# Performance work log

Measured on AMD Instinct MI355X. Metric: run time of the kernel, lower is better.

The kernel has to match this reference:

```python
import jax, jax.numpy as jnp
import numpy as np

N_NODES = 100000
IN_CH, HID_CH, OUT_CH = 128, 256, 128
N_EDGES = 1600000


def setup_inputs() -> dict:
    key = jax.random.key(0)
    ks = jax.random.split(key, 12)
    x = jax.random.normal(ks[0], (N_NODES, IN_CH), dtype=jnp.float32)
    edge_index = jax.random.randint(ks[1], (2, N_EDGES), 0, N_NODES, dtype=jnp.int32)
    s1 = 1.0 / np.sqrt(IN_CH)
    s2 = 1.0 / np.sqrt(HID_CH)
    return {
        "x": x,
        "edge_index": edge_index,
        "eps1": jnp.zeros((), jnp.float32),
        "W1a": jax.random.uniform(ks[2], (IN_CH, HID_CH), jnp.float32, -s1, s1),
        "b1a": jax.random.uniform(ks[3], (HID_CH,), jnp.float32, -s1, s1),
        "W1b": jax.random.uniform(ks[4], (HID_CH, HID_CH), jnp.float32, -s2, s2),
        "b1b": jax.random.uniform(ks[5], (HID_CH,), jnp.float32, -s2, s2),
        "eps2": jnp.zeros((), jnp.float32),
        "W2a": jax.random.uniform(ks[6], (HID_CH, HID_CH), jnp.float32, -s2, s2),
        "b2a": jax.random.uniform(ks[7], (HID_CH,), jnp.float32, -s2, s2),
        "W2b": jax.random.uniform(ks[8], (HID_CH, OUT_CH), jnp.float32, -s2, s2),
        "b2b": jax.random.uniform(ks[9], (OUT_CH,), jnp.float32, -s2, s2),
    }


def _gin_conv(x, src, dst, eps, Wa, ba, Wb, bb):
    # sum-aggregate source features into destinations: [N, d]
    agg = jax.ops.segment_sum(x[src], dst, num_segments=N_NODES)
    h = (1.0 + eps) * x + agg
    h = jax.nn.relu(h @ Wa + ba)
    return h @ Wb + bb


def reference(x, edge_index, eps1, W1a, b1a, W1b, b1b, eps2, W2a, b2a, W2b, b2b):
    src, dst = edge_index[0], edge_index[1]
    h = _gin_conv(x, src, dst, eps1, W1a, b1a, W1b, b1b)
    h = jax.nn.relu(h)
    out = _gin_conv(h, src, dst, eps2, W2a, b2a, W2b, b2b)
    return out
```

## Files before the change

### kernel.cpp

```cpp
#include <hip/hip_runtime.h>

#define N_NODES 100000
#define N_EDGES 1600000
#define NB 782
#define SC_BLK 256

typedef __attribute__((ext_vector_type(8))) short short8;
typedef __attribute__((ext_vector_type(4))) float float4e;

#define GLDS16(g, l)                                                   \
  __builtin_amdgcn_global_load_lds(                                    \
      (const __attribute__((address_space(1))) unsigned int*)(g),      \
      (__attribute__((address_space(3))) unsigned int*)(l), 16, 0, 0)

__device__ __forceinline__ unsigned short f2bf(float f) {
  unsigned u = __float_as_uint(f);
  u += 0x7FFFu + ((u >> 16) & 1u);
  return (unsigned short)(u >> 16);
}
__device__ __forceinline__ float bf2f(unsigned short h) {
  return __uint_as_float(((unsigned)h) << 16);
}

__global__ __launch_bounds__(256) void histA_k(const int* __restrict__ dst,
                                               int* __restrict__ bh, int nE) {
  __shared__ int h[NB];
  const int blk = blockIdx.x, tid = threadIdx.x;
  for (int b = tid; b < NB; b += 256) h[b] = 0;
  __syncthreads();
  const int epb = (nE + SC_BLK - 1) / SC_BLK;
  const int i1 = min(blk * epb + epb, nE);
  for (int i = blk * epb + tid; i < i1; i += 256)
    atomicAdd(&h[dst[i] >> 7], 1);
  __syncthreads();
  for (int b = tid; b < NB; b += 256) bh[b * SC_BLK + blk] = h[b];
}

__global__ __launch_bounds__(256) void scanW_k(int* __restrict__ bh,
                                               int* __restrict__ tot) {
  const int b = blockIdx.x * 4 + (threadIdx.x >> 6);
  const int lane = threadIdx.x & 63;
  if (b >= NB) return;
  const int base = b * SC_BLK + lane * 4;
  int v[4];
#pragma unroll
  for (int j = 0; j < 4; ++j) v[j] = bh[base + j];
  int ls = v[0] + v[1] + v[2] + v[3];
  int x = ls;
  for (int off = 1; off < 64; off <<= 1) {
    int y = __shfl_up(x, off);
    if (lane >= off) x += y;
  }
  int run = x - ls;
#pragma unroll
  for (int j = 0; j < 4; ++j) {
    int t = v[j];
    bh[base + j] = run;
    run += t;
  }
  if (lane == 63) tot[b] = run;
}

__global__ __launch_bounds__(1024) void scanB2_k(const int* __restrict__ tot,
                                                 int* __restrict__ bucketStart) {
  __shared__ int sm[1024];
  const int tid = threadIdx.x;
  int v = (tid < NB) ? tot[tid] : 0;
  sm[tid] = v;
  __syncthreads();
  for (int off = 1; off < 1024; off <<= 1) {
    int t = (tid >= off) ? sm[tid - off] : 0;
    __syncthreads();
    sm[tid] += t;
    __syncthreads();
  }
  if (tid < NB) bucketStart[tid] = sm[tid] - v;
  if (tid == NB - 1) bucketStart[NB] = sm[tid];
}

__global__ __launch_bounds__(256) void scatter2_k(
    const int* __restrict__ src, const int* __restrict__ dst,
    const int* __restrict__ bucketStart, const int* __restrict__ bh,
    unsigned int* __restrict__ packed, int nE) {
  __shared__ int cur[NB];
  const int blk = blockIdx.x, tid = threadIdx.x;
  for (int b = tid; b < NB; b += 256)
    cur[b] = bucketStart[b] + bh[b * SC_BLK + blk];
  __syncthreads();
  const int epb = (nE + SC_BLK - 1) / SC_BLK;
  const int i1 = min(blk * epb + epb, nE);
  for (int i = blk * epb + tid; i < i1; i += 256) {
    int d = dst[i];
    int s = src[i];
    int p = atomicAdd(&cur[d >> 7], 1);
    packed[p] = ((unsigned)s << 7) | (unsigned)(d & 127);
  }
}

__global__ __launch_bounds__(256) void fillB_k(
    const int* __restrict__ bucketStart, const unsigned int* __restrict__ packed,
    int* __restrict__ rowEnd, int* __restrict__ sortedSrc, int nNodes) {
  __shared__ int cnt[128];
  __shared__ int cur[128];
  const int b = blockIdx.x;
  const int tid = threadIdx.x;
  const int s0 = bucketStart[b];
  const int ne = bucketStart[b + 1] - s0;
  if (tid < 128) cnt[tid] = 0;
  __syncthreads();
  for (int i = tid; i < ne; i += 256)
    atomicAdd(&cnt[packed[s0 + i] & 127u], 1);
  __syncthreads();
  int v = (tid < 128) ? cnt[tid] : 0;
  for (int off = 1; off < 128; off <<= 1) {
    int t = (tid < 128 && tid >= off) ? cnt[tid - off] : 0;
    __syncthreads();
    if (tid < 128) cnt[tid] += t;
    __syncthreads();
  }
  if (tid < 128) {
    cur[tid] = s0 + cnt[tid] - v;
    int node = b * 128 + tid;
    if (node < nNodes) rowEnd[node] = s0 + cnt[tid];
  }
  __syncthreads();
  for (int i = tid; i < ne; i += 256) {
    unsigned p = packed[s0 + i];
    int idx = atomicAdd(&cur[p & 127u], 1);
    sortedSrc[idx] = (int)(p >> 7);
  }
}

__global__ __launch_bounds__(256) void wprep_k(
    const float* __restrict__ W, unsigned short* __restrict__ th,
    unsigned short* __restrict__ tl, int K, int N) {
  int i = blockIdx.x * blockDim.x + threadIdx.x;
  if (i < K * N) {
    int k = i / N, n = i % N;
    float v = W[i];
    unsigned short h = f2bf(v);
    unsigned short l = f2bf(v - bf2f(h));
    th[(long)n * K + k] = h;
    tl[(long)n * K + k] = l;
  }
}

__global__ __launch_bounds__(256) void xprep_k(const float* __restrict__ x,
                                               unsigned short* __restrict__ xh,
                                               int n) {
  int i = blockIdx.x * blockDim.x + threadIdx.x;
  if (i < n) xh[i] = f2bf(x[i]);
}

template <bool XF32>
__global__ __launch_bounds__(256) void agg_s_k(
    const unsigned short* __restrict__ feat_h, const float* __restrict__ xf,
    const unsigned short* __restrict__ xh, const unsigned short* __restrict__ xl,
    const float* __restrict__ epsp, const int* __restrict__ rowEnd,
    const int* __restrict__ sortedSrc, unsigned short* __restrict__ oh,
    unsigned short* __restrict__ ol, int M, int S, int off) {
  constexpr int V = 2;
  const int lane = threadIdx.x & 63;
  const int w = (int)((blockIdx.x * blockDim.x + threadIdx.x) >> 6);
  if (w >= M) return;
  const int start = w ? rowEnd[w - 1] : 0;
  const int end = rowEnd[w];
  const int c0 = lane * V + off;

  float acc[V] = {};
  int e = start;
  for (; e + 8 <= end; e += 8) {
    int si[8];
#pragma unroll
    for (int q = 0; q < 8; ++q) si[q] = sortedSrc[e + q];
    ushort2 t[8];
#pragma unroll
    for (int q = 0; q < 8; ++q)
      t[q] = *(const ushort2*)(feat_h + (long)si[q] * S + c0);
#pragma unroll
    for (int q = 0; q < 8; ++q) {
      acc[0] += bf2f(t[q].x);
      acc[1] += bf2f(t[q].y);
    }
  }
  for (; e + 4 <= end; e += 4) {
    int s0 = sortedSrc[e + 0];
    int s1 = sortedSrc[e + 1];
    int s2 = sortedSrc[e + 2];
    int s3 = sortedSrc[e + 3];
    ushort2 a = *(const ushort2*)(feat_h + (long)s0 * S + c0);
    ushort2 b = *(const ushort2*)(feat_h + (long)s1 * S + c0);
    ushort2 c = *(const ushort2*)(feat_h + (long)s2 * S + c0);
    ushort2 d = *(const ushort2*)(feat_h + (long)s3 * S + c0);
    acc[0] += bf2f(a.x) + bf2f(b.x) + bf2f(c.x) + bf2f(d.x);
    acc[1] += bf2f(a.y) + bf2f(b.y) + bf2f(c.y) + bf2f(d.y);
  }
  for (; e < end; ++e) {
    ushort2 a = *(const ushort2*)(feat_h + (long)sortedSrc[e] * S + c0);
    acc[0] += bf2f(a.x);
    acc[1] += bf2f(a.y);
  }

  const float s = 1.0f + epsp[0];
  float xv[V];
  if constexpr (XF32) {
#pragma unroll
    for (int v = 0; v < V; ++v) xv[v] = xf[(long)w * S + c0 + v];
  } else {
#pragma unroll
    for (int v = 0; v < V; ++v)
      xv[v] = bf2f(xh[(long)w * S + c0 + v]) + bf2f(xl[(long)w * S + c0 + v]);
  }

  unsigned short hv[V], lv[V];
#pragma unroll
  for (int v = 0; v < V; ++v) {
    float res = fmaf(s, xv[v], acc[v]);
    hv[v] = f2bf(res);
    lv[v] = f2bf(res - bf2f(hv[v]));
  }
  *(ushort2*)&oh[(long)w * S + c0] = make_ushort2(hv[0], hv[1]);
  *(ushort2*)&ol[(long)w * S + c0] = make_ushort2(lv[0], lv[1]);
}

__device__ __forceinline__ short8 lds_rd(const unsigned short* base, int r,
                                         int q) {
  int L = r * 64 + q * 16;
  int P = L ^ (((L >> 7) & 7) << 4);
  return *(const short8*)((const char*)base + P);
}

template <bool RELU, bool HILO>
__global__ __launch_bounds__(256, 2) void gemm128_k(
    const unsigned short* __restrict__ Ah, const unsigned short* __restrict__ Al,
    const unsigned short* __restrict__ Bth, const unsigned short* __restrict__ Btl,
    const float* __restrict__ bias, float* __restrict__ outf,
    unsigned short* __restrict__ oh, unsigned short* __restrict__ ol,
    int M, int K, int NOUT) {
  __shared__ unsigned short Ash[128 * 32];
  __shared__ unsigned short Asl[128 * 32];
  __shared__ unsigned short Bsh[128 * 32];
  __shared__ unsigned short Bsl[128 * 32];

  const int tid = threadIdx.x;
  const int lane = tid & 63;
  const int wave = tid >> 6;
  const int l15 = lane & 15;
  const int quad = lane >> 4;
  const int wm = wave >> 1;
  const int wn = wave & 1;
  const int m0 = blockIdx.x * 128;
  const int n0 = blockIdx.y * 128;

  float4e acc[4][4];
#pragma unroll
  for (int i = 0; i < 4; ++i)
#pragma unroll
    for (int j = 0; j < 4; ++j) acc[i][j] = 0.0f;

  for (int k0 = 0; k0 < K; k0 += 32) {
#pragma unroll
    for (int h = 0; h < 2; ++h) {
      int c = h * 256 + tid;
      int P = c * 16;
      int L = P ^ (((P >> 7) & 7) << 4);
      int r = L >> 6;
      int q = (L >> 4) & 3;
      if (m0 + r < M) {
        long ga = (long)(m0 + r) * K + k0 + q * 8;
        GLDS16(Ah + ga, Ash + c * 8);
        GLDS16(Al + ga, Asl + c * 8);
      }
      long gb = (long)(n0 + r) * K + k0 + q * 8;
      GLDS16(Bth + gb, Bsh + c * 8);
      GLDS16(Btl + gb, Bsl + c * 8);
    }
    __syncthreads();

    short8 ah[4], al[4];
#pragma unroll
    for (int mi = 0; mi < 4; ++mi) {
      ah[mi] = lds_rd(Ash, wm * 64 + mi * 16 + l15, quad);
      al[mi] = lds_rd(Asl, wm * 64 + mi * 16 + l15, quad);
    }
#pragma unroll
    for (int ni = 0; ni < 4; ++ni) {
      short8 bh = lds_rd(Bsh, wn * 64 + ni * 16 + l15, quad);
      short8 bl = lds_rd(Bsl, wn * 64 + ni * 16 + l15, quad);
#pragma unroll
      for (int mi = 0; mi < 4; ++mi) {
        acc[mi][ni] =
            __builtin_amdgcn_mfma_f32_16x16x32_bf16(ah[mi], bh, acc[mi][ni], 0, 0, 0);
        acc[mi][ni] =
            __builtin_amdgcn_mfma_f32_16x16x32_bf16(ah[mi], bl, acc[mi][ni], 0, 0, 0);
        acc[mi][ni] =
            __builtin_amdgcn_mfma_f32_16x16x32_bf16(al[mi], bh, acc[mi][ni], 0, 0, 0);
      }
    }
    __syncthreads();
  }

#pragma unroll
  for (int mi = 0; mi < 4; ++mi) {
#pragma unroll
    for (int ni = 0; ni < 4; ++ni) {
      int col = n0 + wn * 64 + ni * 16 + l15;
      float bj = bias[col];
      int rbase = m0 + wm * 64 + mi * 16 + quad * 4;
#pragma unroll
      for (int r = 0; r < 4; ++r) {
        int row = rbase + r;
        if (row < M) {
          float v = acc[mi][ni][r] + bj;
          if constexpr (RELU) v = fmaxf(v, 0.0f);
          if constexpr (HILO) {
            unsigned short h = f2bf(v);
            oh[(long)row * NOUT + col] = h;
            ol[(long)row * NOUT + col] = f2bf(v - bf2f(h));
          } else {
            outf[(long)row * NOUT + col] = v;
          }
        }
      }
    }
  }
}

extern "C" void kernel_launch(void* const* d_in, const int* in_sizes, int n_in,
                              void* d_out, int out_size, void* d_ws, size_t ws_size,
                              hipStream_t stream) {
  const float* x    = (const float*)d_in[0];
  const int*   ei   = (const int*)d_in[1];
  const float* eps1 = (const float*)d_in[2];
  const float* W1a  = (const float*)d_in[3];
  const float* b1a  = (const float*)d_in[4];
  const float* W1b  = (const float*)d_in[5];
  const float* b1b  = (const float*)d_in[6];
  const float* eps2 = (const float*)d_in[7];
  const float* W2a  = (const float*)d_in[8];
  const float* b2a  = (const float*)d_in[9];
  const float* W2b  = (const float*)d_in[10];
  const float* b2b  = (const float*)d_in[11];
  float* out = (float*)d_out;

  const int* srcp = ei;
  const int* dstp = ei + N_EDGES;

  char* ws = (char*)d_ws;
  const size_t SZ = (size_t)N_NODES * 256 * sizeof(float);
  char* P1 = ws;
  char* P2 = ws + SZ;

  unsigned short* C1h = (unsigned short*)P1;
  unsigned short* C1l = C1h + (size_t)N_NODES * 128;
  unsigned short* xh  = C1l + (size_t)N_NODES * 128;
  unsigned short* T1h = (unsigned short*)P2;
  unsigned short* T1l = T1h + (size_t)N_NODES * 256;
  unsigned short* Hh = (unsigned short*)P1;
  unsigned short* Hl = Hh + (size_t)N_NODES * 256;
  unsigned short* C2h = (unsigned short*)P2;
  unsigned short* C2l = C2h + (size_t)N_NODES * 256;
  unsigned short* T2h = (unsigned short*)P1;
  unsigned short* T2l = T2h + (size_t)N_NODES * 256;
  unsigned short* W2bh = (unsigned short*)P2;
  unsigned short* W2bl = W2bh + 128 * 256;

  char* ob = (char*)d_out;
  int* rowEnd    = (int*)(ob + 400 * 1024);
  int* sortedSrc = (int*)(ob + 800 * 1024);
  size_t wofs = 7340032;
  unsigned short* W1ah = (unsigned short*)(ob + wofs);
  unsigned short* W1al = W1ah + 256 * 128;
  unsigned short* W1bh = (unsigned short*)(ob + wofs + 2 * 65536);
  unsigned short* W1bl = W1bh + 256 * 256;
  unsigned short* W2ah = (unsigned short*)(ob + wofs + 2 * 65536 + 2 * 131072);
  unsigned short* W2al = W2ah + 256 * 256;
  unsigned int* packed = (unsigned int*)(ob + 16 * 1024 * 1024);
  int* bucketStart = (int*)(ob + 28 * 1024 * 1024);
  int* bucketTot   = (int*)(ob + 28 * 1024 * 1024 + 8192);
  int* blockHist   = (int*)(ob + 30 * 1024 * 1024);

  dim3 blk(256);
  dim3 gAgg((N_NODES + 3) / 4);
  dim3 gW1((128 * 256 + 255) / 256);
  dim3 gW2((256 * 256 + 255) / 256);
  dim3 gXp((N_NODES * 128 + 255) / 256);
  dim3 gGemm2((N_NODES + 127) / 128, 2);
  dim3 gGemm1((N_NODES + 127) / 128, 1);

  histA_k<<<dim3(SC_BLK), blk, 0, stream>>>(dstp, blockHist, N_EDGES);
  scanW_k<<<dim3((NB + 3) / 4), blk, 0, stream>>>(blockHist, bucketTot);
  scanB2_k<<<1, dim3(1024), 0, stream>>>(bucketTot, bucketStart);
  scatter2_k<<<dim3(SC_BLK), blk, 0, stream>>>(srcp, dstp, bucketStart,
                                               blockHist, packed, N_EDGES);
  fillB_k<<<dim3(NB), blk, 0, stream>>>(bucketStart, packed, rowEnd, sortedSrc,
                                        N_NODES);
  xprep_k<<<gXp, blk, 0, stream>>>(x, xh, N_NODES * 128);
  wprep_k<<<gW1, blk, 0, stream>>>(W1a, W1ah, W1al, 128, 256);
  wprep_k<<<gW2, blk, 0, stream>>>(W1b, W1bh, W1bl, 256, 256);
  wprep_k<<<gW2, blk, 0, stream>>>(W2a, W2ah, W2al, 256, 256);

  agg_s_k<true><<<gAgg, blk, 0, stream>>>(
      xh, x, nullptr, nullptr, eps1, rowEnd, sortedSrc, C1h, C1l, N_NODES, 128, 0);
  gemm128_k<true, true><<<gGemm2, blk, 0, stream>>>(
      C1h, C1l, W1ah, W1al, b1a, nullptr, T1h, T1l, N_NODES, 128, 256);
  gemm128_k<true, true><<<gGemm2, blk, 0, stream>>>(
      T1h, T1l, W1bh, W1bl, b1b, nullptr, Hh, Hl, N_NODES, 256, 256);

  agg_s_k<false><<<gAgg, blk, 0, stream>>>(
      Hh, nullptr, Hh, Hl, eps2, rowEnd, sortedSrc, C2h, C2l, N_NODES, 256, 0);
  agg_s_k<false><<<gAgg, blk, 0, stream>>>(
      Hh, nullptr, Hh, Hl, eps2, rowEnd, sortedSrc, C2h, C2l, N_NODES, 256, 128);
  gemm128_k<true, true><<<gGemm2, blk, 0, stream>>>(
      C2h, C2l, W2ah, W2al, b2a, nullptr, T2h, T2l, N_NODES, 256, 256);
  wprep_k<<<gW1, blk, 0, stream>>>(W2b, W2bh, W2bl, 256, 128);
  gemm128_k<false, false><<<gGemm1, blk, 0, stream>>>(
      T2h, T2l, W2bh, W2bl, b2b, out, nullptr, nullptr, N_NODES, 256, 128);
}
```

Baseline: 662.7 us.

## Double-buffer GEMM LDS tiles to overlap global loads with MFMA

The GEMM kernel now keeps two LDS buffers per operand and issues the global-to-LDS loads for the next K tile before computing on the current one, using explicit vmcnt waits and raw barriers. The goal is to hide global load latency behind the bf16 hi/lo MFMA work. Out-of-range A rows are clamped instead of skipped so every thread issues the same number of loads, which keeps the vmcnt count fixed. The cost is twice the LDS (64KB per block), which may lower occupancy against the launch_bounds(256,2) target, and it relies on the hand-written waitcnt being correct.

```diff
diff --git a/kernel.cpp b/kernel.cpp
--- a/kernel.cpp
+++ b/kernel.cpp
@@ -12,6 +12,9 @@
   __builtin_amdgcn_global_load_lds(                                    \
       (const __attribute__((address_space(1))) unsigned int*)(g),      \
       (__attribute__((address_space(3))) unsigned int*)(l), 16, 0, 0)
+
+#define WAITVM_(N) asm volatile("s_waitcnt vmcnt(" #N ")" ::: "memory")
+#define WAITVM(N) WAITVM_(N)
 
 __device__ __forceinline__ unsigned short f2bf(float f) {
   unsigned u = __float_as_uint(f);
@@ -237,10 +240,10 @@
     const float* __restrict__ bias, float* __restrict__ outf,
     unsigned short* __restrict__ oh, unsigned short* __restrict__ ol,
     int M, int K, int NOUT) {
-  __shared__ unsigned short Ash[128 * 32];
-  __shared__ unsigned short Asl[128 * 32];
-  __shared__ unsigned short Bsh[128 * 32];
-  __shared__ unsigned short Bsl[128 * 32];
+  __shared__ unsigned short Ash[2][128 * 32];
+  __shared__ unsigned short Asl[2][128 * 32];
+  __shared__ unsigned short Bsh[2][128 * 32];
+  __shared__ unsigned short Bsl[2][128 * 32];
 
   const int tid = threadIdx.x;
   const int lane = tid & 63;
@@ -258,7 +261,7 @@
 #pragma unroll
     for (int j = 0; j < 4; ++j) acc[i][j] = 0.0f;
 
-  for (int k0 = 0; k0 < K; k0 += 32) {
+  auto stage = [&](int buf, int k0) {
 #pragma unroll
     for (int h = 0; h < 2; ++h) {
       int c = h * 256 + tid;
@@ -266,27 +269,40 @@
       int L = P ^ (((P >> 7) & 7) << 4);
       int r = L >> 6;
       int q = (L >> 4) & 3;
-      if (m0 + r < M) {
-        long ga = (long)(m0 + r) * K + k0 + q * 8;
-        GLDS16(Ah + ga, Ash + c * 8);
-        GLDS16(Al + ga, Asl + c * 8);
-      }
+      int ra = min(m0 + r, M - 1);
+      long ga = (long)ra * K + k0 + q * 8;
+      GLDS16(Ah + ga, &Ash[buf][c * 8]);
+      GLDS16(Al + ga, &Asl[buf][c * 8]);
       long gb = (long)(n0 + r) * K + k0 + q * 8;
-      GLDS16(Bth + gb, Bsh + c * 8);
-      GLDS16(Btl + gb, Bsl + c * 8);
-    }
-    __syncthreads();
+      GLDS16(Bth + gb, &Bsh[buf][c * 8]);
+      GLDS16(Btl + gb, &Bsl[buf][c * 8]);
+    }
+  };
+
+  const int nt = K >> 5;
+  stage(0, 0);
+
+  for (int t = 0; t < nt; ++t) {
+    const int cur = t & 1;
+    if (t + 1 < nt) {
+      stage(cur ^ 1, (t + 1) * 32);
+      WAITVM(8);
+    } else {
+      WAITVM(0);
+    }
+    __builtin_amdgcn_s_barrier();
+    __builtin_amdgcn_sched_barrier(0);
 
     short8 ah[4], al[4];
 #pragma unroll
     for (int mi = 0; mi < 4; ++mi) {
-      ah[mi] = lds_rd(Ash, wm * 64 + mi * 16 + l15, quad);
-      al[mi] = lds_rd(Asl, wm * 64 + mi * 16 + l15, quad);
+      ah[mi] = lds_rd(&Ash[cur][0], wm * 64 + mi * 16 + l15, quad);
+      al[mi] = lds_rd(&Asl[cur][0], wm * 64 + mi * 16 + l15, quad);
     }
 #pragma unroll
     for (int ni = 0; ni < 4; ++ni) {
-      short8 bh = lds_rd(Bsh, wn * 64 + ni * 16 + l15, quad);
-      short8 bl = lds_rd(Bsl, wn * 64 + ni * 16 + l15, quad);
+      short8 bh = lds_rd(&Bsh[cur][0], wn * 64 + ni * 16 + l15, quad);
+      short8 bl = lds_rd(&Bsl[cur][0], wn * 64 + ni * 16 + l15, quad);
 #pragma unroll
       for (int mi = 0; mi < 4; ++mi) {
         acc[mi][ni] =
@@ -297,7 +313,8 @@
             __builtin_amdgcn_mfma_f32_16x16x32_bf16(al[mi], bh, acc[mi][ni], 0, 0, 0);
       }
     }
-    __syncthreads();
+    __builtin_amdgcn_s_barrier();
+    __builtin_amdgcn_sched_barrier(0);
   }
 
 #pragma unroll
```

New measurement: 718.1 us. 1.08x slower.

## Fuse each GIN MLP's two GEMMs into one kernel keeping hidden tile in LDS

Applied to the files above, without the earlier changes.

Each pair of back-to-back GEMMs in a GIN MLP now runs as one kernel. The 128x256 hidden tile is written as hi/lo bf16 into LDS and consumed directly by the second GEMM, so the T1/T2 intermediates no longer round-trip through global memory and two launches are removed. Weights are now read straight from global memory (through cache) instead of being staged in LDS. The kernel uses about 144KB of LDS at one block per CU, which lowers occupancy and may stall on the uncoalesced per-lane weight loads.

```diff
diff --git a/kernel.cpp b/kernel.cpp
--- a/kernel.cpp
+++ b/kernel.cpp
@@ -230,17 +230,22 @@
   return *(const short8*)((const char*)base + P);
 }
 
-template <bool RELU, bool HILO>
-__global__ __launch_bounds__(256, 2) void gemm128_k(
+#define MFMA_BF16 __builtin_amdgcn_mfma_f32_16x16x32_bf16
+
+template <int K1, int NF2, bool RELU2, bool HILO2>
+__global__ __launch_bounds__(256, 1) void gemm_fused_k(
     const unsigned short* __restrict__ Ah, const unsigned short* __restrict__ Al,
-    const unsigned short* __restrict__ Bth, const unsigned short* __restrict__ Btl,
-    const float* __restrict__ bias, float* __restrict__ outf,
-    unsigned short* __restrict__ oh, unsigned short* __restrict__ ol,
-    int M, int K, int NOUT) {
+    const unsigned short* __restrict__ B1th, const unsigned short* __restrict__ B1tl,
+    const float* __restrict__ bias1,
+    const unsigned short* __restrict__ B2th, const unsigned short* __restrict__ B2tl,
+    const float* __restrict__ bias2,
+    float* __restrict__ outf, unsigned short* __restrict__ oh,
+    unsigned short* __restrict__ ol, int M) {
+  constexpr int N2 = NF2 * 32;
   __shared__ unsigned short Ash[128 * 32];
   __shared__ unsigned short Asl[128 * 32];
-  __shared__ unsigned short Bsh[128 * 32];
-  __shared__ unsigned short Bsl[128 * 32];
+  __shared__ unsigned short Th[8 * 128 * 32];
+  __shared__ unsigned short Tl[8 * 128 * 32];
 
   const int tid = threadIdx.x;
   const int lane = tid & 63;
@@ -250,75 +255,119 @@
   const int wm = wave >> 1;
   const int wn = wave & 1;
   const int m0 = blockIdx.x * 128;
-  const int n0 = blockIdx.y * 128;
-
-  float4e acc[4][4];
+
+  {
+    float4e acc1[4][8];
+#pragma unroll
+    for (int i = 0; i < 4; ++i)
+#pragma unroll
+      for (int j = 0; j < 8; ++j) acc1[i][j] = 0.0f;
+
+    for (int k0 = 0; k0 < K1; k0 += 32) {
+#pragma unroll
+      for (int h = 0; h < 2; ++h) {
+        int c = h * 256 + tid;
+        int P = c * 16;
+        int L = P ^ (((P >> 7) & 7) << 4);
+        int r = L >> 6;
+        int q = (L >> 4) & 3;
+        int ra = min(m0 + r, M - 1);
+        long ga = (long)ra * K1 + k0 + q * 8;
+        GLDS16(Ah + ga, &Ash[c * 8]);
+        GLDS16(Al + ga, &Asl[c * 8]);
+      }
+      __syncthreads();
+
+      short8 ah[4], al[4];
+#pragma unroll
+      for (int mi = 0; mi < 4; ++mi) {
+        ah[mi] = lds_rd(Ash, wm * 64 + mi * 16 + l15, quad);
+        al[mi] = lds_rd(Asl, wm * 64 + mi * 16 + l15, quad);
+      }
+#pragma unroll
+      for (int ni = 0; ni < 8; ++ni) {
+        int n = wn * 128 + ni * 16 + l15;
+        short8 bh = *(const short8*)(B1th + (long)n * K1 + k0 + quad * 8);
+        short8 bl = *(const short8*)(B1tl + (long)n * K1 + k0 + quad * 8);
+#pragma unroll
+        for (int mi = 0; mi < 4; ++mi) {
+          acc1[mi][ni] = MFMA_BF16(ah[mi], bh, acc1[mi][ni], 0, 0, 0);
+          acc1[mi][ni] = MFMA_BF16(ah[mi], bl, acc1[mi][ni], 0, 0, 0);
+          acc1[mi][ni] = MFMA_BF16(al[mi], bh, acc1[mi][ni], 0, 0, 0);
+        }
+      }
+      __syncthreads();
+    }
+
+#pragma unroll
+    for (int ni = 0; ni < 8; ++ni) {
+      int col = wn * 128 + ni * 16 + l15;
+      float bj = bias1[col];
+      int sb = (col >> 5) * 4096;
+      int c5 = (col & 31) * 2;
+#pragma unroll
+      for (int mi = 0; mi < 4; ++mi) {
+#pragma unroll
+        for (int r = 0; r < 4; ++r) {
+          int row = wm * 64 + mi * 16 + quad * 4 + r;
+          float v = fmaxf(acc1[mi][ni][r] + bj, 0.0f);
+          unsigned short hv = f2bf(v);
+          unsigned short lv = f2bf(v - bf2f(hv));
+          int L = row * 64 + c5;
+          int P = L ^ (((L >> 7) & 7) << 4);
+          *(unsigned short*)((char*)(Th + sb) + P) = hv;
+          *(unsigned short*)((char*)(Tl + sb) + P) = lv;
+        }
+      }
+    }
+  }
+  __syncthreads();
+
+  float4e acc2[4][NF2];
 #pragma unroll
   for (int i = 0; i < 4; ++i)
 #pragma unroll
-    for (int j = 0; j < 4; ++j) acc[i][j] = 0.0f;
-
-  for (int k0 = 0; k0 < K; k0 += 32) {
-#pragma unroll
-    for (int h = 0; h < 2; ++h) {
-      int c = h * 256 + tid;
-      int P = c * 16;
-      int L = P ^ (((P >> 7) & 7) << 4);
-      int r = L >> 6;
-      int q = (L >> 4) & 3;
-      if (m0 + r < M) {
-        long ga = (long)(m0 + r) * K + k0 + q * 8;
-        GLDS16(Ah + ga, Ash + c * 8);
-        GLDS16(Al + ga, Asl + c * 8);
-      }
-      long gb = (long)(n0 + r) * K + k0 + q * 8;
-      GLDS16(Bth + gb, Bsh + c * 8);
-      GLDS16(Btl + gb, Bsl + c * 8);
-    }
-    __syncthreads();
-
-    short8 ah[4], al[4];
+    for (int j = 0; j < NF2; ++j) acc2[i][j] = 0.0f;
+
+  for (int kt = 0; kt < 8; ++kt) {
+    short8 ah2[4], al2[4];
 #pragma unroll
     for (int mi = 0; mi < 4; ++mi) {
-      ah[mi] = lds_rd(Ash, wm * 64 + mi * 16 + l15, quad);
-      al[mi] = lds_rd(Asl, wm * 64 + mi * 16 + l15, quad);
-    }
-#pragma unroll
-    for (int ni = 0; ni < 4; ++ni) {
-      short8 bh = lds_rd(Bsh, wn * 64 + ni * 16 + l15, quad);
-      short8 bl = lds_rd(Bsl, wn * 64 + ni * 16 + l15, quad);
+      ah2[mi] = lds_rd(Th + kt * 4096, wm * 64 + mi * 16 + l15, quad);
+      al2[mi] = lds_rd(Tl + kt * 4096, wm * 64 + mi * 16 + l15, quad);
+    }
+#pragma unroll
+    for (int ni = 0; ni < NF2; ++ni) {
+      int n = wn * (NF2 * 16) + ni * 16 + l15;
+      short8 bh = *(const short8*)(B2th + (long)n * 256 + kt * 32 + quad * 8);
+      short8 bl = *(const short8*)(B2tl + (long)n * 256 + kt * 32 + quad * 8);
 #pragma unroll
       for (int mi = 0; mi < 4; ++mi) {
-        acc[mi][ni] =
-            __builtin_amdgcn_mfma_f32_16x16x32_bf16(ah[mi], bh, acc[mi][ni], 0, 0, 0);
-        acc[mi][ni] =
-            __builtin_amdgcn_mfma_f32_16x16x32_bf16(ah[mi], bl, acc[mi][ni], 0, 0, 0);
-        acc[mi][ni] =
-            __builtin_amdgcn_mfma_f32_16x16x32_bf16(al[mi], bh, acc[mi][ni], 0, 0, 0);
-      }
-    }
-    __syncthreads();
-  }
-
-#pragma unroll
-  for (int mi = 0; mi < 4; ++mi) {
-#pragma unroll
-    for (int ni = 0; ni < 4; ++ni) {
-      int col = n0 + wn * 64 + ni * 16 + l15;
-      float bj = bias[col];
-      int rbase = m0 + wm * 64 + mi * 16 + quad * 4;
+        acc2[mi][ni] = MFMA_BF16(ah2[mi], bh, acc2[mi][ni], 0, 0, 0);
+        acc2[mi][ni] = MFMA_BF16(ah2[mi], bl, acc2[mi][ni], 0, 0, 0);
+        acc2[mi][ni] = MFMA_BF16(al2[mi], bh, acc2[mi][ni], 0, 0, 0);
+      }
+    }
+  }
+
+#pragma unroll
+  for (int ni = 0; ni < NF2; ++ni) {
+    int col = wn * (NF2 * 16) + ni * 16 + l15;
+    float bj = bias2[col];
+#pragma unroll
+    for (int mi = 0; mi < 4; ++mi) {
 #pragma unroll
       for (int r = 0; r < 4; ++r) {
-        int row = rbase + r;
+        int row = m0 + wm * 64 + mi * 16 + quad * 4 + r;
         if (row < M) {
-          float v = acc[mi][ni][r] + bj;
-          if constexpr (RELU) v = fmaxf(v, 0.0f);
-          if constexpr (HILO) {
-            unsigned short h = f2bf(v);
-            oh[(long)row * NOUT + col] = h;
-            ol[(long)row * NOUT + col] = f2bf(v - bf2f(h));
+          float v = acc2[mi][ni][r] + bj;
+          if constexpr (RELU2) v = fmaxf(v, 0.0f);
+          if constexpr (HILO2) {
+            unsigned short hv = f2bf(v);
+            oh[(long)row * N2 + col] = hv;
+            ol[(long)row * N2 + col] = f2bf(v - bf2f(hv));
           } else {
-            outf[(long)row * NOUT + col] = v;
+            outf[(long)row * N2 + col] = v;
           }
         }
       }
@@ -354,15 +403,13 @@
   unsigned short* C1h = (unsigned short*)P1;
   unsigned short* C1l = C1h + (size_t)N_NODES * 128;
   unsigned short* xh  = C1l + (size_t)N_NODES * 128;
-  unsigned short* T1h = (unsigned short*)P2;
-  unsigned short* T1l = T1h + (size_t)N_NODES * 256;
-  unsigned short* Hh = (unsigned short*)P1;
-  unsigned short* Hl = Hh + (size_t)N_NODES * 256;
-  unsigned short* C2h = (unsigned short*)P2;
+  unsigned short* Hh  = (unsigned short*)P2;
+  unsigned short* Hl  = Hh + (size_t)N_NODES * 256;
+  unsigned short* C2h = (unsigned short*)P1;
   unsigned short* C2l = C2h + (size_t)N_NODES * 256;
-  unsigned short* T2h = (unsigned short*)P1;
-  unsigned short* T2l = T2h + (size_t)N_NODES * 256;
-  unsigned short* W2bh = (unsigned short*)P2;
+  unsigned short* W2ah = (unsigned short*)P2;
+  unsigned short* W2al = W2ah + 256 * 256;
+  unsigned short* W2bh = W2al + 256 * 256;
   unsigned short* W2bl = W2bh + 128 * 256;
 
   char* ob = (char*)d_out;
@@ -373,8 +420,6 @@
   unsigned short* W1al = W1ah + 256 * 128;
   unsigned short* W1bh = (unsigned short*)(ob + wofs + 2 * 65536);
   unsigned short* W1bl = W1bh + 256 * 256;
-  unsigned short* W2ah = (unsigned short*)(ob + wofs + 2 * 65536 + 2 * 131072);
-  unsigned short* W2al = W2ah + 256 * 256;
   unsigned int* packed = (unsigned int*)(ob + 16 * 1024 * 1024);
   int* bucketStart = (int*)(ob + 28 * 1024 * 1024);
   int* bucketTot   = (int*)(ob + 28 * 1024 * 1024 + 8192);
@@ -385,8 +430,7 @@
   dim3 gW1((128 * 256 + 255) / 256);
   dim3 gW2((256 * 256 + 255) / 256);
   dim3 gXp((N_NODES * 128 + 255) / 256);
-  dim3 gGemm2((N_NODES + 127) / 128, 2);
-  dim3 gGemm1((N_NODES + 127) / 128, 1);
+  dim3 gFused((N_NODES + 127) / 128);
 
   histA_k<<<dim3(SC_BLK), blk, 0, stream>>>(dstp, blockHist, N_EDGES);
   scanW_k<<<dim3((NB + 3) / 4), blk, 0, stream>>>(blockHist, bucketTot);
@@ -398,22 +442,19 @@
   xprep_k<<<gXp, blk, 0, stream>>>(x, xh, N_NODES * 128);
   wprep_k<<<gW1, blk, 0, stream>>>(W1a, W1ah, W1al, 128, 256);
   wprep_k<<<gW2, blk, 0, stream>>>(W1b, W1bh, W1bl, 256, 256);
-  wprep_k<<<gW2, blk, 0, stream>>>(W2a, W2ah, W2al, 256, 256);
 
   agg_s_k<true><<<gAgg, blk, 0, stream>>>(
       xh, x, nullptr, nullptr, eps1, rowEnd, sortedSrc, C1h, C1l, N_NODES, 128, 0);
-  gemm128_k<true, true><<<gGemm2, blk, 0, stream>>>(
-      C1h, C1l, W1ah, W1al, b1a, nullptr, T1h, T1l, N_NODES, 128, 256);
-  gemm128_k<true, true><<<gGemm2, blk, 0, stream>>>(
-      T1h, T1l, W1bh, W1bl, b1b, nullptr, Hh, Hl, N_NODES, 256, 256);
+  gemm_fused_k<128, 8, true, true><<<gFused, blk, 0, stream>>>(
+      C1h, C1l, W1ah, W1al, b1a, W1bh, W1bl, b1b, nullptr, Hh, Hl, N_NODES);
 
   agg_s_k<false><<<gAgg, blk, 0, stream>>>(
       Hh, nullptr, Hh, Hl, eps2, rowEnd, sortedSrc, C2h, C2l, N_NODES, 256, 0);
   agg_s_k<false><<<gAgg, blk, 0, stream>>>(
       Hh, nullptr, Hh, Hl, eps2, rowEnd, sortedSrc, C2h, C2l, N_NODES, 256, 128);
-  gemm128_k<true, true><<<gGemm2, blk, 0, stream>>>(
-      C2h, C2l, W2ah, W2al, b2a, nullptr, T2h, T2l, N_NODES, 256, 256);
+  wprep_k<<<gW2, blk, 0, stream>>>(W2a, W2ah, W2al, 256, 256);
   wprep_k<<<gW1, blk, 0, stream>>>(W2b, W2bh, W2bl, 256, 128);
-  gemm128_k<false, false><<<gGemm1, blk, 0, stream>>>(
-      T2h, T2l, W2bh, W2bl, b2b, out, nullptr, nullptr, N_NODES, 256, 128);
-}
+  gemm_fused_k<256, 4, false, false><<<gFused, blk, 0, stream>>>(
+      C2h, C2l, W2ah, W2al, b2a, W2bh, W2bl, b2b, out, nullptr, nullptr,
+      N_NODES);
+}
```

Result: slower. 865.6 us (+30.6%).

## Widen GEMM tile to full output width and read weights directly from global

Applied to the files above, without the earlier changes.

Each GEMM block now computes all output columns (256 or 128) for its 128-row tile, so the activation tile is loaded once instead of once per column block. The weight tiles are no longer staged in LDS; each wave reads B fragments straight from global memory, relying on cache because the weights are small and shared by every block. Row bounds checks are replaced by clamping to the last row. The wider tile doubles accumulator registers per thread (NF=8), which may hurt occupancy, and the uncoalesced direct global B reads add latency inside the MFMA loop.

```diff
diff --git a/kernel.cpp b/kernel.cpp
--- a/kernel.cpp
+++ b/kernel.cpp
@@ -230,17 +230,18 @@
   return *(const short8*)((const char*)base + P);
 }
 
-template <bool RELU, bool HILO>
-__global__ __launch_bounds__(256, 2) void gemm128_k(
+#define MFMA_BF16 __builtin_amdgcn_mfma_f32_16x16x32_bf16
+
+template <int NF, bool RELU, bool HILO>
+__global__ __launch_bounds__(256, 2) void gemmW_k(
     const unsigned short* __restrict__ Ah, const unsigned short* __restrict__ Al,
     const unsigned short* __restrict__ Bth, const unsigned short* __restrict__ Btl,
     const float* __restrict__ bias, float* __restrict__ outf,
     unsigned short* __restrict__ oh, unsigned short* __restrict__ ol,
-    int M, int K, int NOUT) {
+    int M, int K) {
+  constexpr int N = NF * 32;
   __shared__ unsigned short Ash[128 * 32];
   __shared__ unsigned short Asl[128 * 32];
-  __shared__ unsigned short Bsh[128 * 32];
-  __shared__ unsigned short Bsl[128 * 32];
 
   const int tid = threadIdx.x;
   const int lane = tid & 63;
@@ -250,13 +251,12 @@
   const int wm = wave >> 1;
   const int wn = wave & 1;
   const int m0 = blockIdx.x * 128;
-  const int n0 = blockIdx.y * 128;
-
-  float4e acc[4][4];
+
+  float4e acc[4][NF];
 #pragma unroll
   for (int i = 0; i < 4; ++i)
 #pragma unroll
-    for (int j = 0; j < 4; ++j) acc[i][j] = 0.0f;
+    for (int j = 0; j < NF; ++j) acc[i][j] = 0.0f;
 
   for (int k0 = 0; k0 < K; k0 += 32) {
 #pragma unroll
@@ -266,14 +266,10 @@
       int L = P ^ (((P >> 7) & 7) << 4);
       int r = L >> 6;
       int q = (L >> 4) & 3;
-      if (m0 + r < M) {
-        long ga = (long)(m0 + r) * K + k0 + q * 8;
-        GLDS16(Ah + ga, Ash + c * 8);
-        GLDS16(Al + ga, Asl + c * 8);
-      }
-      long gb = (long)(n0 + r) * K + k0 + q * 8;
-      GLDS16(Bth + gb, Bsh + c * 8);
-      GLDS16(Btl + gb, Bsl + c * 8);
+      int ra = min(m0 + r, M - 1);
+      long ga = (long)ra * K + k0 + q * 8;
+      GLDS16(Ah + ga, &Ash[c * 8]);
+      GLDS16(Al + ga, &Asl[c * 8]);
     }
     __syncthreads();
 
@@ -284,28 +280,26 @@
       al[mi] = lds_rd(Asl, wm * 64 + mi * 16 + l15, quad);
     }
 #pragma unroll
-    for (int ni = 0; ni < 4; ++ni) {
-      short8 bh = lds_rd(Bsh, wn * 64 + ni * 16 + l15, quad);
-      short8 bl = lds_rd(Bsl, wn * 64 + ni * 16 + l15, quad);
+    for (int ni = 0; ni < NF; ++ni) {
+      int n = wn * (NF * 16) + ni * 16 + l15;
+      short8 bh = *(const short8*)(Bth + (long)n * K + k0 + quad * 8);
+      short8 bl = *(const short8*)(Btl + (long)n * K + k0 + quad * 8);
 #pragma unroll
       for (int mi = 0; mi < 4; ++mi) {
-        acc[mi][ni] =
-            __builtin_amdgcn_mfma_f32_16x16x32_bf16(ah[mi], bh, acc[mi][ni], 0, 0, 0);
-        acc[mi][ni] =
-            __builtin_amdgcn_mfma_f32_16x16x32_bf16(ah[mi], bl, acc[mi][ni], 0, 0, 0);
-        acc[mi][ni] =
-            __builtin_amdgcn_mfma_f32_16x16x32_bf16(al[mi], bh, acc[mi][ni], 0, 0, 0);
+        acc[mi][ni] = MFMA_BF16(ah[mi], bh, acc[mi][ni], 0, 0, 0);
+        acc[mi][ni] = MFMA_BF16(ah[mi], bl, acc[mi][ni], 0, 0, 0);
+        acc[mi][ni] = MFMA_BF16(al[mi], bh, acc[mi][ni], 0, 0, 0);
       }
     }
     __syncthreads();
   }
 
 #pragma unroll
-  for (int mi = 0; mi < 4; ++mi) {
-#pragma unroll
-    for (int ni = 0; ni < 4; ++ni) {
-      int col = n0 + wn * 64 + ni * 16 + l15;
-      float bj = bias[col];
+  for (int ni = 0; ni < NF; ++ni) {
+    int col = wn * (NF * 16) + ni * 16 + l15;
+    float bj = bias[col];
+#pragma unroll
+    for (int mi = 0; mi < 4; ++mi) {
       int rbase = m0 + wm * 64 + mi * 16 + quad * 4;
 #pragma unroll
       for (int r = 0; r < 4; ++r) {
@@ -315,10 +309,10 @@
           if constexpr (RELU) v = fmaxf(v, 0.0f);
           if constexpr (HILO) {
             unsigned short h = f2bf(v);
-            oh[(long)row * NOUT + col] = h;
-            ol[(long)row * NOUT + col] = f2bf(v - bf2f(h));
+            oh[(long)row * N + col] = h;
+            ol[(long)row * N + col] = f2bf(v - bf2f(h));
           } else {
-            outf[(long)row * NOUT + col] = v;
+            outf[(long)row * N + col] = v;
           }
         }
       }
@@ -385,8 +379,7 @@
   dim3 gW1((128 * 256 + 255) / 256);
   dim3 gW2((256 * 256 + 255) / 256);
   dim3 gXp((N_NODES * 128 + 255) / 256);
-  dim3 gGemm2((N_NODES + 127) / 128, 2);
-  dim3 gGemm1((N_NODES + 127) / 128, 1);
+  dim3 gGemm((N_NODES + 127) / 128);
 
   histA_k<<<dim3(SC_BLK), blk, 0, stream>>>(dstp, blockHist, N_EDGES);
   scanW_k<<<dim3((NB + 3) / 4), blk, 0, stream>>>(blockHist, bucketTot);
@@ -402,18 +395,18 @@
 
   agg_s_k<true><<<gAgg, blk, 0, stream>>>(
       xh, x, nullptr, nullptr, eps1, rowEnd, sortedSrc, C1h, C1l, N_NODES, 128, 0);
-  gemm128_k<true, true><<<gGemm2, blk, 0, stream>>>(
-      C1h, C1l, W1ah, W1al, b1a, nullptr, T1h, T1l, N_NODES, 128, 256);
-  gemm128_k<true, true><<<gGemm2, blk, 0, stream>>>(
-      T1h, T1l, W1bh, W1bl, b1b, nullptr, Hh, Hl, N_NODES, 256, 256);
+  gemmW_k<8, true, true><<<gGemm, blk, 0, stream>>>(
+      C1h, C1l, W1ah, W1al, b1a, nullptr, T1h, T1l, N_NODES, 128);
+  gemmW_k<8, true, true><<<gGemm, blk, 0, stream>>>(
+      T1h, T1l, W1bh, W1bl, b1b, nullptr, Hh, Hl, N_NODES, 256);
 
   agg_s_k<false><<<gAgg, blk, 0, stream>>>(
       Hh, nullptr, Hh, Hl, eps2, rowEnd, sortedSrc, C2h, C2l, N_NODES, 256, 0);
   agg_s_k<false><<<gAgg, blk, 0, stream>>>(
       Hh, nullptr, Hh, Hl, eps2, rowEnd, sortedSrc, C2h, C2l, N_NODES, 256, 128);
-  gemm128_k<true, true><<<gGemm2, blk, 0, stream>>>(
-      C2h, C2l, W2ah, W2al, b2a, nullptr, T2h, T2l, N_NODES, 256, 256);
+  gemmW_k<8, true, true><<<gGemm, blk, 0, stream>>>(
+      C2h, C2l, W2ah, W2al, b2a, nullptr, T2h, T2l, N_NODES, 256);
   wprep_k<<<gW1, blk, 0, stream>>>(W2b, W2bh, W2bl, 256, 128);
-  gemm128_k<false, false><<<gGemm1, blk, 0, stream>>>(
-      T2h, T2l, W2bh, W2bl, b2b, out, nullptr, nullptr, N_NODES, 256, 128);
-}
+  gemmW_k<4, false, false><<<gGemm, blk, 0, stream>>>(
+      T2h, T2l, W2bh, W2bl, b2b, out, nullptr, nullptr, N_NODES, 256);
+}
```

After: 833.6 us. 1.26x slower.
